# Performance work log

Measured on AMD Instinct MI355X. Metric: run time of the kernel, lower is better.

The kernel has to match this reference:

```python
import jax, jax.numpy as jnp
import numpy as np

B, N, D, U = 8, 2048, 512, 512

def setup_inputs() -> dict:
    key = jax.random.key(0)
    ks = jax.random.split(key, 7)
    s = 1.0 / np.sqrt(D)
    return {
        "inputs": jax.random.normal(ks[0], (B, N, D), dtype=jnp.float32),
        "Wq": jax.random.normal(ks[1], (D, U), dtype=jnp.float32) * s,
        "bq": jnp.zeros((U,), dtype=jnp.float32),
        "Wk": jax.random.normal(ks[2], (D, U), dtype=jnp.float32) * s,
        "bk": jnp.zeros((U,), dtype=jnp.float32),
        "Wv": jax.random.normal(ks[3], (D, U), dtype=jnp.float32) * s,
        "bv": jnp.zeros((U,), dtype=jnp.float32),
    }

def reference(inputs, Wq, bq, Wk, bk, Wv, bv):
    # Dense projections (Keras Dense: x @ W + b)
    Q = inputs @ Wq + bq  # [B, N, U]
    K = inputs @ Wk + bk  # [B, N, U]
    V = inputs @ Wv + bv  # [B, N, U]
    # NOTE: original module has NO 1/sqrt(d) scaling
    scores = jnp.einsum("bnu,bmu->bnm", Q, K)  # [B, N, N]
    attn = jax.nn.softmax(scores, axis=-1)
    return jnp.einsum("bnm,bmu->bnu", attn, V)  # [B, N, U]
```

## Files before the change

kernel.cpp:

```cpp
#include <hip/hip_runtime.h>


typedef _Float16 f16;
typedef _Float16 f16x4 __attribute__((ext_vector_type(4)));
typedef _Float16 f16x8 __attribute__((ext_vector_type(8)));
typedef float f32x4 __attribute__((ext_vector_type(4)));
typedef short s16x8 __attribute__((ext_vector_type(8)));
typedef unsigned short u16;

#define OFS 96.0f

__device__ __forceinline__ void stage16(const void* g, void* lds_uniform) {
    __builtin_amdgcn_global_load_lds(
        (const __attribute__((address_space(1))) void*)g,
        (__attribute__((address_space(3))) void*)lds_uniform,
        16, 0, 0);
}

__device__ __forceinline__ u16 f2bf(float f) {
    unsigned u = __builtin_bit_cast(unsigned, f);
    u = (u + 0x7FFF + ((u >> 16) & 1)) >> 16;
    return (u16)u;
}
__device__ __forceinline__ float bf2f(u16 b) {
    return __builtin_bit_cast(float, (unsigned)b << 16);
}

__global__ __launch_bounds__(256) void prep_fused(
    const float* __restrict__ X,
    const float* __restrict__ Wq, const float* __restrict__ Wk,
    const float* __restrict__ Wv,
    const float* __restrict__ bq, const float* __restrict__ bk,
    const float* __restrict__ bv,
    f16* __restrict__ X16, f16* __restrict__ Wt, float* __restrict__ biases,
    float* __restrict__ rowsum) {
    __shared__ float t[32][33];
    const int bid = blockIdx.x, tid = threadIdx.x;
    if (bid < 8192) {
        int i = (bid * 256 + tid) * 4;
        float4 v = *(const float4*)(X + i);
        f16x4 o;
        o[0] = (f16)v.x; o[1] = (f16)v.y; o[2] = (f16)v.z; o[3] = (f16)v.w;
        *(f16x4*)(X16 + i) = o;
    } else if (bid < 8960) {
        int id = bid - 8192;
        int z = id >> 8, rem = id & 255;
        int u0 = (rem & 15) * 32, d0 = (rem >> 4) * 32;
        const float* W = (z == 0) ? Wq : (z == 1 ? Wk : Wv);
        f16* outp = Wt + (size_t)z * 262144;
        int tx = tid & 31, ty = tid >> 5;
#pragma unroll
        for (int r = 0; r < 4; r++)
            t[ty + 8 * r][tx] = W[(size_t)(d0 + ty + 8 * r) * 512 + u0 + tx];
        __syncthreads();
#pragma unroll
        for (int r = 0; r < 4; r++)
            outp[(size_t)(u0 + ty + 8 * r) * 512 + d0 + tx] = (f16)t[tx][ty + 8 * r];
    } else if (bid == 8960) {
#pragma unroll
        for (int j = 0; j < 6; j++) {
            int i = j * 256 + tid;
            float v = (i < 512) ? bq[i] : (i < 1024) ? bk[i - 512] : bv[i - 1024];
            biases[i] = v;
        }
    } else {
        int id = bid - 8961;
        float4 z4 = {0.f, 0.f, 0.f, 0.f};
        ((float4*)rowsum)[id * 256 + tid] = z4;
    }
}

template <int MODE>
__device__ __forceinline__ void gemm_core(
    const u16* __restrict__ A, int lda,
    const u16* __restrict__ Bt, int ldb,
    int m0, int n0, int K,
    const float* __restrict__ bias, float* __restrict__ rs,
    void* __restrict__ Cv, int ldc,
    u16* As, u16* Bs) {
    __shared__ float rowbuf[128];

    const int tid = threadIdx.x;
    const int wid = tid >> 6, lane = tid & 63;

    if (MODE == 2 || MODE == 4) {
        if (tid < 128) rowbuf[tid] = (MODE == 2 ? bias : rs)[m0 + tid];
    }

    const int schunk = (lane & 7) ^ ((lane >> 3) & 7);
    const u16* gA = A + (size_t)(m0 + wid * 32 + (lane >> 3)) * lda + schunk * 8;
    const u16* gB = Bt + (size_t)(n0 + wid * 32 + (lane >> 3)) * ldb + schunk * 8;
    u16* ldsA = As + (wid * 32) * 64;
    u16* ldsB = Bs + (wid * 32) * 64;

    const int wr = wid >> 1, wc = wid & 1;
    const int frow = lane & 15;
    const int f7 = frow & 7;
    const int c_lo = (lane >> 4) ^ f7;
    const int c_hi = ((lane >> 4) | 4) ^ f7;
    const u16* fA_lo = As + (wr * 64 + frow) * 64 + c_lo * 8;
    const u16* fA_hi = As + (wr * 64 + frow) * 64 + c_hi * 8;
    const u16* fB_lo = Bs + (wc * 64 + frow) * 64 + c_lo * 8;
    const u16* fB_hi = Bs + (wc * 64 + frow) * 64 + c_hi * 8;

    f32x4 acc[4][4] = {};

    for (int kt = 0; kt < K; kt += 64) {
#pragma unroll
        for (int j = 0; j < 4; j++)
            stage16(gA + (size_t)(j * 8) * lda, ldsA + (j * 8) * 64);
#pragma unroll
        for (int j = 0; j < 4; j++)
            stage16(gB + (size_t)(j * 8) * ldb, ldsB + (j * 8) * 64);
        gA += 64; gB += 64;
        __syncthreads();

#pragma unroll
        for (int half = 0; half < 2; half++) {
            const u16* pA = half ? fA_hi : fA_lo;
            const u16* pB = half ? fB_hi : fB_lo;
            if (MODE == 4) {
                s16x8 af[4], bf[4];
#pragma unroll
                for (int i = 0; i < 4; i++) af[i] = *(const s16x8*)(pA + i * 16 * 64);
#pragma unroll
                for (int i = 0; i < 4; i++) bf[i] = *(const s16x8*)(pB + i * 16 * 64);
#pragma unroll
                for (int mi = 0; mi < 4; mi++)
#pragma unroll
                    for (int ni = 0; ni < 4; ni++)
                        acc[mi][ni] = __builtin_amdgcn_mfma_f32_16x16x32_bf16(
                            af[mi], bf[ni], acc[mi][ni], 0, 0, 0);
            } else {
                f16x8 af[4], bf[4];
#pragma unroll
                for (int i = 0; i < 4; i++) af[i] = *(const f16x8*)(const f16*)(pA + i * 16 * 64);
#pragma unroll
                for (int i = 0; i < 4; i++) bf[i] = *(const f16x8*)(const f16*)(pB + i * 16 * 64);
#pragma unroll
                for (int mi = 0; mi < 4; mi++)
#pragma unroll
                    for (int ni = 0; ni < 4; ni++)
                        acc[mi][ni] = __builtin_amdgcn_mfma_f32_16x16x32_f16(
                            af[mi], bf[ni], acc[mi][ni], 0, 0, 0);
            }
        }
        __syncthreads();
    }

    const int crow0 = m0 + wr * 64 + ((lane >> 4) << 2);
    const int ccol0 = n0 + wc * 64 + (lane & 15);

    if (MODE == 1) {
        f16* C = (f16*)Cv;
#pragma unroll
        for (int mi = 0; mi < 4; mi++)
#pragma unroll
            for (int ni = 0; ni < 4; ni++) {
                float cb = bias[ccol0 + ni * 16];
#pragma unroll
                for (int r = 0; r < 4; r++)
                    C[(size_t)(crow0 + mi * 16 + r) * ldc + ccol0 + ni * 16] =
                        (f16)(acc[mi][ni][r] + cb);
            }
    } else if (MODE == 2) {
        u16* C = (u16*)Cv;
#pragma unroll
        for (int mi = 0; mi < 4; mi++)
#pragma unroll
            for (int ni = 0; ni < 4; ni++)
#pragma unroll
                for (int r = 0; r < 4; r++) {
                    float rb = rowbuf[crow0 + mi * 16 + r - m0];
                    C[(size_t)(crow0 + mi * 16 + r) * ldc + ccol0 + ni * 16] =
                        f2bf(acc[mi][ni][r] + rb);
                }
    } else {
        float* C = (float*)Cv;
#pragma unroll
        for (int mi = 0; mi < 4; mi++) {
            float inv[4];
#pragma unroll
            for (int r = 0; r < 4; r++)
                inv[r] = 1.0f / rowbuf[crow0 + mi * 16 + r - m0];
#pragma unroll
            for (int ni = 0; ni < 4; ni++)
#pragma unroll
                for (int r = 0; r < 4; r++)
                    C[(size_t)(crow0 + mi * 16 + r) * ldc + ccol0 + ni * 16] =
                        acc[mi][ni][r] * inv[r];
        }
    }
}

__global__ __launch_bounds__(256) void proj_fused(
    const u16* __restrict__ X16, const u16* __restrict__ Wt,
    const float* __restrict__ biases,
    u16* __restrict__ QK, u16* __restrict__ Vt) {
    __shared__ __align__(16) u16 As[128 * 64];
    __shared__ __align__(16) u16 Bs[128 * 64];
    const int bid = blockIdx.x;
    if (bid < 1024) {
        int z = bid >> 9, rem = bid & 511;
        int bx = rem & 127, by = rem >> 7;
        gemm_core<1>(X16, 512, Wt + (size_t)z * 262144, 512,
                     bx * 128, by * 128, 512,
                     biases + z * 512, nullptr,
                     QK + (size_t)z * 8388608, 512, As, Bs);
    } else {
        int id = bid - 1024;
        int bz = id & 7, rem = id >> 3;
        int bx = rem & 3, by = rem >> 2;
        gemm_core<2>(Wt + (size_t)2 * 262144, 512,
                     X16 + (size_t)bz * 1048576, 512,
                     bx * 128, by * 128, 512,
                     biases + 1024, nullptr,
                     Vt + (size_t)bz * 1048576, 2048, As, Bs);
    }
}

__global__ __launch_bounds__(256, 2) void score_gemm(
    const u16* __restrict__ Q, const u16* __restrict__ Kk,
    u16* __restrict__ P, float* __restrict__ rowsum) {
    __shared__ __align__(16) u16 As[256 * 64];
    __shared__ __align__(16) u16 Bs[128 * 64];

    const int i = blockIdx.x;
    const int z = i & 7, y = (i >> 3) & 15, x = i >> 7;
    const int m0 = x * 256, n0 = y * 128;
    const u16* A = Q + (size_t)z * 1048576;
    const u16* Bt = Kk + (size_t)z * 1048576;
    u16* C = P + (size_t)z * 4194304;
    float* rs = rowsum + z * 2048;

    const int tid = threadIdx.x;
    const int wid = tid >> 6, lane = tid & 63;

    const int schunk = (lane & 7) ^ ((lane >> 3) & 7);
    const u16* gA = A + (size_t)(m0 + wid * 64 + (lane >> 3)) * 512 + schunk * 8;
    u16* ldsA = As + (wid * 64) * 64;
    const u16* gB = Bt + (size_t)(n0 + wid * 32 + (lane >> 3)) * 512 + schunk * 8;
    u16* ldsB = Bs + (wid * 32) * 64;

    const int wr = wid >> 1, wc = wid & 1;
    const int frow = lane & 15;
    const int f7 = frow & 7;
    const int c_lo = (lane >> 4) ^ f7;
    const int c_hi = ((lane >> 4) | 4) ^ f7;
    const u16* fA_lo = As + (wr * 128 + frow) * 64 + c_lo * 8;
    const u16* fA_hi = As + (wr * 128 + frow) * 64 + c_hi * 8;
    const u16* fB_lo = Bs + (wc * 64 + frow) * 64 + c_lo * 8;
    const u16* fB_hi = Bs + (wc * 64 + frow) * 64 + c_hi * 8;

    f32x4 acc[8][4] = {};

    for (int kt = 0; kt < 512; kt += 64) {
#pragma unroll
        for (int j = 0; j < 8; j++)
            stage16(gA + (size_t)(j * 8) * 512, ldsA + (j * 8) * 64);
#pragma unroll
        for (int j = 0; j < 4; j++)
            stage16(gB + (size_t)(j * 8) * 512, ldsB + (j * 8) * 64);
        gA += 64; gB += 64;
        __syncthreads();

#pragma unroll
        for (int half = 0; half < 2; half++) {
            const u16* pA = half ? fA_hi : fA_lo;
            const u16* pB = half ? fB_hi : fB_lo;
            f16x8 bf[4];
#pragma unroll
            for (int ni = 0; ni < 4; ni++)
                bf[ni] = *(const f16x8*)(const f16*)(pB + ni * 16 * 64);
#pragma unroll
            for (int mig = 0; mig < 2; mig++) {
                f16x8 af[4];
#pragma unroll
                for (int j = 0; j < 4; j++)
                    af[j] = *(const f16x8*)(const f16*)(pA + ((mig * 4 + j) * 16) * 64);
#pragma unroll
                for (int j = 0; j < 4; j++)
#pragma unroll
                    for (int ni = 0; ni < 4; ni++)
                        acc[mig * 4 + j][ni] = __builtin_amdgcn_mfma_f32_16x16x32_f16(
                            af[j], bf[ni], acc[mig * 4 + j][ni], 0, 0, 0);
            }
        }
        __syncthreads();
    }

    const int crow0 = m0 + wr * 128 + ((lane >> 4) << 2);
    const int ccol0 = n0 + wc * 64 + (lane & 15);
#pragma unroll
    for (int mi = 0; mi < 8; mi++)
#pragma unroll
        for (int r = 0; r < 4; r++) {
            float rsum = 0.0f;
#pragma unroll
            for (int ni = 0; ni < 4; ni++) {
                u16 b = f2bf(__expf(acc[mi][ni][r] - OFS));
                C[(size_t)(crow0 + mi * 16 + r) * 2048 + ccol0 + ni * 16] = b;
                rsum += bf2f(b);
            }
#pragma unroll
            for (int o = 1; o < 16; o <<= 1)
                rsum += __shfl_xor(rsum, o, 64);
            if ((lane & 15) == 0)
                atomicAdd(rs + crow0 + mi * 16 + r, rsum);
        }
}

__global__ __launch_bounds__(256) void pv_gemm(
    const u16* __restrict__ P, const u16* __restrict__ Vt,
    float* __restrict__ rowsum, float* __restrict__ out) {
    __shared__ __align__(16) u16 As[128 * 64];
    __shared__ __align__(16) u16 Bs[128 * 64];
    const int i = blockIdx.x;
    const int z = i & 7, y = (i >> 3) & 3, x = i >> 5;
    gemm_core<4>(P + (size_t)z * 4194304, 2048,
                 Vt + (size_t)z * 1048576, 2048,
                 x * 128, y * 128, 2048,
                 nullptr, rowsum + z * 2048,
                 out + (size_t)z * 1048576, 512, As, Bs);
}


extern "C" void kernel_launch(void* const* d_in, const int* in_sizes, int n_in,
                              void* d_out, int out_size, void* d_ws, size_t ws_size,
                              hipStream_t stream) {
    const float* X  = (const float*)d_in[0];
    const float* Wq = (const float*)d_in[1];
    const float* bq = (const float*)d_in[2];
    const float* Wk = (const float*)d_in[3];
    const float* bk = (const float*)d_in[4];
    const float* Wv = (const float*)d_in[5];
    const float* bv = (const float*)d_in[6];
    float* out = (float*)d_out;
    char* ws = (char*)d_ws;

    f16*   X16    = (f16*)ws;
    f16*   Wt     = (f16*)(ws + 16777216);
    float* biases = (float*)(ws + 18350080);
    u16*   QK     = (u16*)(ws + 18356224);
    u16*   Vt     = (u16*)(ws + 51910656);
    u16*   P      = (u16*)(ws + 68687872);
    float* rowsum = (float*)(ws + 135796736);

    prep_fused<<<8977, 256, 0, stream>>>(X, Wq, Wk, Wv, bq, bk, bv,
                                         X16, Wt, biases, rowsum);

    proj_fused<<<1536, 256, 0, stream>>>((const u16*)X16, (const u16*)Wt,
                                         biases, QK, Vt);

    score_gemm<<<1024, 256, 0, stream>>>(QK, QK + (size_t)8388608, P, rowsum);

    pv_gemm<<<512, 256, 0, stream>>>(P, Vt, rowsum, out);
}
```

Baseline: 214.6 us.

## Shrink score GEMM to single-wave 64x64 tiles without block barriers

The score GEMM moves from 256-thread blocks computing 256x128 tiles to 64-thread single-wave blocks computing 64x64 tiles, launched as 8192 blocks. Because each block is one wave, the __syncthreads barriers are replaced by a wait on outstanding memory counters, and the LDS footprint per block shrinks. The aim is to remove barrier stalls and raise occupancy and scheduling flexibility. The cost is much lower operand reuse: each Q and K tile is loaded from global memory several times more often. There is also no double buffering, so loads and MFMAs within a wave do not overlap.

```diff
diff --git a/kernel.cpp b/kernel.cpp
--- a/kernel.cpp
+++ b/kernel.cpp
@@ -219,80 +219,69 @@
     }
 }
 
-__global__ __launch_bounds__(256, 2) void score_gemm(
+__global__ __launch_bounds__(64) void score_gemm(
     const u16* __restrict__ Q, const u16* __restrict__ Kk,
     u16* __restrict__ P, float* __restrict__ rowsum) {
-    __shared__ __align__(16) u16 As[256 * 64];
-    __shared__ __align__(16) u16 Bs[128 * 64];
+    __shared__ __align__(16) u16 As[64 * 64];
+    __shared__ __align__(16) u16 Bs[64 * 64];
 
     const int i = blockIdx.x;
-    const int z = i & 7, y = (i >> 3) & 15, x = i >> 7;
-    const int m0 = x * 256, n0 = y * 128;
+    const int z = i & 7, y = (i >> 3) & 31, x = i >> 8;
+    const int m0 = x * 64, n0 = y * 64;
     const u16* A = Q + (size_t)z * 1048576;
     const u16* Bt = Kk + (size_t)z * 1048576;
     u16* C = P + (size_t)z * 4194304;
     float* rs = rowsum + z * 2048;
 
-    const int tid = threadIdx.x;
-    const int wid = tid >> 6, lane = tid & 63;
+    const int lane = threadIdx.x;
 
     const int schunk = (lane & 7) ^ ((lane >> 3) & 7);
-    const u16* gA = A + (size_t)(m0 + wid * 64 + (lane >> 3)) * 512 + schunk * 8;
-    u16* ldsA = As + (wid * 64) * 64;
-    const u16* gB = Bt + (size_t)(n0 + wid * 32 + (lane >> 3)) * 512 + schunk * 8;
-    u16* ldsB = Bs + (wid * 32) * 64;
-
-    const int wr = wid >> 1, wc = wid & 1;
+    const u16* gA = A + (size_t)(m0 + (lane >> 3)) * 512 + schunk * 8;
+    const u16* gB = Bt + (size_t)(n0 + (lane >> 3)) * 512 + schunk * 8;
+
     const int frow = lane & 15;
     const int f7 = frow & 7;
     const int c_lo = (lane >> 4) ^ f7;
     const int c_hi = ((lane >> 4) | 4) ^ f7;
-    const u16* fA_lo = As + (wr * 128 + frow) * 64 + c_lo * 8;
-    const u16* fA_hi = As + (wr * 128 + frow) * 64 + c_hi * 8;
-    const u16* fB_lo = Bs + (wc * 64 + frow) * 64 + c_lo * 8;
-    const u16* fB_hi = Bs + (wc * 64 + frow) * 64 + c_hi * 8;
-
-    f32x4 acc[8][4] = {};
+    const u16* fA_lo = As + frow * 64 + c_lo * 8;
+    const u16* fA_hi = As + frow * 64 + c_hi * 8;
+    const u16* fB_lo = Bs + frow * 64 + c_lo * 8;
+    const u16* fB_hi = Bs + frow * 64 + c_hi * 8;
+
+    f32x4 acc[4][4] = {};
 
     for (int kt = 0; kt < 512; kt += 64) {
 #pragma unroll
         for (int j = 0; j < 8; j++)
-            stage16(gA + (size_t)(j * 8) * 512, ldsA + (j * 8) * 64);
-#pragma unroll
-        for (int j = 0; j < 4; j++)
-            stage16(gB + (size_t)(j * 8) * 512, ldsB + (j * 8) * 64);
+            stage16(gA + (size_t)(j * 8) * 512, As + (j * 8) * 64);
+#pragma unroll
+        for (int j = 0; j < 8; j++)
+            stage16(gB + (size_t)(j * 8) * 512, Bs + (j * 8) * 64);
         gA += 64; gB += 64;
-        __syncthreads();
+        __builtin_amdgcn_s_waitcnt(0);
 
 #pragma unroll
         for (int half = 0; half < 2; half++) {
             const u16* pA = half ? fA_hi : fA_lo;
             const u16* pB = half ? fB_hi : fB_lo;
-            f16x8 bf[4];
-#pragma unroll
-            for (int ni = 0; ni < 4; ni++)
-                bf[ni] = *(const f16x8*)(const f16*)(pB + ni * 16 * 64);
-#pragma unroll
-            for (int mig = 0; mig < 2; mig++) {
-                f16x8 af[4];
-#pragma unroll
-                for (int j = 0; j < 4; j++)
-                    af[j] = *(const f16x8*)(const f16*)(pA + ((mig * 4 + j) * 16) * 64);
-#pragma unroll
-                for (int j = 0; j < 4; j++)
-#pragma unroll
-                    for (int ni = 0; ni < 4; ni++)
-                        acc[mig * 4 + j][ni] = __builtin_amdgcn_mfma_f32_16x16x32_f16(
-                            af[j], bf[ni], acc[mig * 4 + j][ni], 0, 0, 0);
-            }
-        }
-        __syncthreads();
-    }
-
-    const int crow0 = m0 + wr * 128 + ((lane >> 4) << 2);
-    const int ccol0 = n0 + wc * 64 + (lane & 15);
-#pragma unroll
-    for (int mi = 0; mi < 8; mi++)
+            f16x8 af[4], bf[4];
+#pragma unroll
+            for (int j = 0; j < 4; j++) af[j] = *(const f16x8*)(const f16*)(pA + j * 16 * 64);
+#pragma unroll
+            for (int j = 0; j < 4; j++) bf[j] = *(const f16x8*)(const f16*)(pB + j * 16 * 64);
+#pragma unroll
+            for (int mi = 0; mi < 4; mi++)
+#pragma unroll
+                for (int ni = 0; ni < 4; ni++)
+                    acc[mi][ni] = __builtin_amdgcn_mfma_f32_16x16x32_f16(
+                        af[mi], bf[ni], acc[mi][ni], 0, 0, 0);
+        }
+    }
+
+    const int crow0 = m0 + ((lane >> 4) << 2);
+    const int ccol0 = n0 + (lane & 15);
+#pragma unroll
+    for (int mi = 0; mi < 4; mi++)
 #pragma unroll
         for (int r = 0; r < 4; r++) {
             float rsum = 0.0f;
@@ -352,7 +341,7 @@
     proj_fused<<<1536, 256, 0, stream>>>((const u16*)X16, (const u16*)Wt,
                                          biases, QK, Vt);
 
-    score_gemm<<<1024, 256, 0, stream>>>(QK, QK + (size_t)8388608, P, rowsum);
+    score_gemm<<<8192, 64, 0, stream>>>(QK, QK + (size_t)8388608, P, rowsum);
 
     pv_gemm<<<512, 256, 0, stream>>>(P, Vt, rowsum, out);
 }
```

New measurement: 230.1 us. 1.07x slower.
